# Kernel tuning notes

Measured on AMD Instinct MI355X. Metric: run time of the kernel, lower is better.

Reference implementation:

```python
import jax, jax.numpy as jnp
import numpy as np

IN_F = 512
OUT_F = 512
LMAX = 4
M = (LMAX + 1) ** 2  # 25
BATCH = 4096


def _expand_index():
    # l repeated (2l+1) times: [0, 1,1,1, 2,2,2,2,2, ...]
    return np.concatenate([np.full(2 * l + 1, l, dtype=np.int32) for l in range(LMAX + 1)])


def setup_inputs() -> dict:
    key = jax.random.key(0)
    k1, k2 = jax.random.split(key)
    bound = 1.0 / np.sqrt(IN_F)
    x = jax.random.normal(k1, (BATCH, IN_F * M, 1), dtype=jnp.float32)
    weight = jax.random.uniform(k2, (LMAX + 1, OUT_F, IN_F), dtype=jnp.float32,
                                minval=-bound, maxval=bound)
    bias = jnp.zeros((OUT_F,), dtype=jnp.float32)
    return {"input": x, "weight": weight, "bias": bias}


def reference(input, weight, bias):
    B = input.shape[0]
    idx = jnp.asarray(_expand_index())
    # gather-expand shared per-l weight to per-m weight: [M, out, in]
    w = weight[idx]
    # 'b (i m) n -> b m (i n)' with n=1  => [B, M, in]
    xi = input[..., 0].reshape(B, IN_F, M).transpose(0, 2, 1)
    # batched per-m linear: [B, M, out]
    out = jnp.einsum('bmi,moi->bmo', xi, w)
    # bias added only to the m=0 (l=0 scalar) component
    out = out.at[:, 0, :].add(bias)
    # 'b (m n) o -> b (o m) n' with n=1 => [B, out*M, 1]
    return out.transpose(0, 2, 1).reshape(B, OUT_F * M, 1)
```

## Files before the change

kernel.cpp:

```cpp
#include <hip/hip_runtime.h>
#include <hip/hip_bf16.h>


typedef __bf16 bf16x8 __attribute__((ext_vector_type(8)));
typedef float floatx4 __attribute__((ext_vector_type(4)));
typedef unsigned short ushort_t;
typedef unsigned short ushortx4 __attribute__((ext_vector_type(4)));

#define ROW_F 12800
#define SROW  72
#define LDS_USH (400 * 72)

__device__ __forceinline__ ushort_t f2bf(float f) {
    __hip_bfloat16 h = __float2bfloat16(f);
    return __builtin_bit_cast(ushort_t, h);
}

__global__ void cvt_w_kernel(const float* __restrict__ w, ushort_t* __restrict__ wb) {
    int i = (blockIdx.x * 256 + threadIdx.x) * 4;
    floatx4 v = *reinterpret_cast<const floatx4*>(w + i);
    ushortx4 h;
    h.x = f2bf(v[0]); h.y = f2bf(v[1]); h.z = f2bf(v[2]); h.w = f2bf(v[3]);
    *reinterpret_cast<ushortx4*>(wb + i) = h;
}

__global__ __launch_bounds__(512, 2) void irrep_kernel(
        const float* __restrict__ x, const ushort_t* __restrict__ wb,
        const float* __restrict__ bias, float* __restrict__ out) {
    __shared__ __align__(16) ushort_t Asm[LDS_USH];

    const int tid  = threadIdx.x;
    const int lane = tid & 63;
    const int wv   = tid >> 6;
    const int lr   = lane & 15;
    const int lh   = lane >> 4;

    const int d     = blockIdx.x;
    const int o     = (d & 7) * 128 + (d >> 3);
    const int btile = o >> 2;
    const int ctile = o & 3;
    const int b0    = btile * 16;
    const int o0    = ctile * 128;
    const int ow    = o0 + wv * 16;

    constexpr int LOF[25] = {0,1,1,1,2,2,2,2,2,3,3,3,3,3,3,3,4,4,4,4,4,4,4,4,4};

    floatx4 acc[25];
#pragma unroll
    for (int m = 0; m < 25; ++m) acc[m] = (floatx4){0.f, 0.f, 0.f, 0.f};

    floatx4 vbuf[13];

    auto prefetch = [&](int step) {
#pragma unroll
        for (int it = 0; it < 13; ++it) {
            int idx = tid + it * 512;
            if (idx < 6400) {
                int bb = idx / 400;
                int p  = idx - bb * 400;
                vbuf[it] = *reinterpret_cast<const floatx4*>(
                    x + (size_t)(b0 + bb) * ROW_F + (size_t)step * 1600 + p * 4);
            }
        }
    };

    auto scatter = [&]() {
#pragma unroll
        for (int it = 0; it < 13; ++it) {
            int idx = tid + it * 512;
            if (idx < 6400) {
                int bb = idx / 400;
                int p  = idx - bb * 400;
#pragma unroll
                for (int u = 0; u < 4; ++u) {
                    int q = p * 4 + u;
                    int i = q / 25;
                    int m = q - i * 25;
                    Asm[(m * 16 + bb) * SROW + (i ^ ((m & 7) << 3))] = f2bf(vbuf[it][u]);
                }
            }
        }
    };

    prefetch(0);
#pragma unroll 1
    for (int step = 0; step < 8; ++step) {
        __syncthreads();
        scatter();
        __syncthreads();
        if (step < 7) prefetch(step + 1);
        const int k0 = step * 64;
#pragma unroll
        for (int ks = 0; ks < 2; ++ks) {
            bf16x8 bfr[5];
#pragma unroll
            for (int l = 0; l < 5; ++l)
                bfr[l] = *reinterpret_cast<const bf16x8*>(
                    wb + (size_t)(l * 512 + ow + lr) * 512 + k0 + ks * 32 + lh * 8);
#pragma unroll
            for (int m = 0; m < 25; ++m) {
                const bf16x8 a = *reinterpret_cast<const bf16x8*>(
                    &Asm[(m * 16 + lr) * SROW + ((ks * 32 + lh * 8) ^ ((m & 7) << 3))]);
                acc[m] = __builtin_amdgcn_mfma_f32_16x16x32_bf16(a, bfr[LOF[m]], acc[m], 0, 0, 0);
            }
        }
    }

    {
        float bv = bias[ow + lr];
#pragma unroll
        for (int r = 0; r < 4; ++r) acc[0][r] += bv;
    }

    float* ep = reinterpret_cast<float*>(Asm);
    constexpr int EPROW = 404;
#pragma unroll 1
    for (int pass = 0; pass < 4; ++pass) {
        __syncthreads();
        if ((wv >> 1) == pass) {
            const int half = wv & 1;
            float* epw = ep + half * (16 * EPROW);
#pragma unroll
            for (int m = 0; m < 25; ++m) {
#pragma unroll
                for (int r = 0; r < 4; ++r) {
                    int bl = lh * 4 + r;
                    epw[bl * EPROW + lr * 25 + m] = acc[m][r];
                }
            }
        }
        __syncthreads();
        for (int idx = tid; idx < 3200; idx += 512) {
            int half = idx / 1600;
            int rem  = idx - half * 1600;
            int bl   = rem / 100;
            int q4   = rem - bl * 100;
            floatx4 v = *reinterpret_cast<const floatx4*>(
                &ep[half * (16 * EPROW) + bl * EPROW + q4 * 4]);
            *reinterpret_cast<floatx4*>(
                out + (size_t)(b0 + bl) * ROW_F
                    + (size_t)(o0 + (pass * 2 + half) * 16) * 25 + q4 * 4) = v;
        }
    }
}

extern "C" void kernel_launch(void* const* d_in, const int* in_sizes, int n_in,
                              void* d_out, int out_size, void* d_ws, size_t ws_size,
                              hipStream_t stream) {
    const float* x    = (const float*)d_in[0];
    const float* w    = (const float*)d_in[1];
    const float* bias = (const float*)d_in[2];
    float* outp       = (float*)d_out;
    ushort_t* wb      = (ushort_t*)d_ws;

    cvt_w_kernel<<<1280, 256, 0, stream>>>(w, wb);
    irrep_kernel<<<1024, 512, 0, stream>>>(x, wb, bias, outp);
}
```

Baseline: 272.0 us.

## Restructure irrep GEMM into 10-wave blocks with double-buffered LDS and per-wave m-groups

Splits each block's work so every wave owns a group of five m components across two 16-wide output slices, instead of all 25 m for one slice. Blocks now cover 64 output features with 640 threads and 2048 blocks. The input is staged through a double-buffered LDS tile with a new swizzle and 8-element vector stores, so the next chunk's global loads and scatter overlap the MFMAs, with one barrier per step. The idea is to cut per-wave accumulator registers for higher occupancy and to hide load latency. The cost is that each input tile is loaded twice (once per output half), and the epilogue takes more barriers.

After: 453.3 us. 66.7% more time.

```diff
diff --git a/kernel.cpp b/kernel.cpp
--- a/kernel.cpp
+++ b/kernel.cpp
@@ -2,18 +2,24 @@
 #include <hip/hip_bf16.h>
 
 
-typedef __bf16 bf16x8 __attribute__((ext_vector_type(8)));
+typedef __bf16 bf16x8v __attribute__((ext_vector_type(8)));
 typedef float floatx4 __attribute__((ext_vector_type(4)));
 typedef unsigned short ushort_t;
 typedef unsigned short ushortx4 __attribute__((ext_vector_type(4)));
+typedef unsigned short ushortx8 __attribute__((ext_vector_type(8)));
 
 #define ROW_F 12800
-#define SROW  72
-#define LDS_USH (400 * 72)
+#define BUF_USH 16064
 
 __device__ __forceinline__ ushort_t f2bf(float f) {
     __hip_bfloat16 h = __float2bfloat16(f);
     return __builtin_bit_cast(ushort_t, h);
+}
+
+__device__ __forceinline__ int row_ush(int row) {
+    int m = row >> 4;
+    int t = (m & 8) ? ((15 - m) & 7) : (m & 7);
+    return row * 40 + t * 8;
 }
 
 __global__ void cvt_w_kernel(const float* __restrict__ w, ushort_t* __restrict__ wb) {
@@ -24,123 +30,142 @@
     *reinterpret_cast<ushortx4*>(wb + i) = h;
 }
 
-__global__ __launch_bounds__(512, 2) void irrep_kernel(
+__global__ __launch_bounds__(640, 3) void irrep_kernel(
         const float* __restrict__ x, const ushort_t* __restrict__ wb,
         const float* __restrict__ bias, float* __restrict__ out) {
-    __shared__ __align__(16) ushort_t Asm[LDS_USH];
+    __shared__ __align__(16) ushort_t Asm[2 * BUF_USH];
 
-    const int tid  = threadIdx.x;
-    const int lane = tid & 63;
-    const int wv   = tid >> 6;
-    const int lr   = lane & 15;
-    const int lh   = lane >> 4;
+    const int tid = threadIdx.x, lane = tid & 63, wv = tid >> 6;
+    const int lr = lane & 15, lh = lane >> 4;
 
-    const int d     = blockIdx.x;
-    const int o     = (d & 7) * 128 + (d >> 3);
-    const int btile = o >> 2;
-    const int ctile = o & 3;
-    const int b0    = btile * 16;
-    const int o0    = ctile * 128;
-    const int ow    = o0 + wv * 16;
+    const int hw = blockIdx.x;
+    const int sib = (hw >> 3) & 7;
+    const int btile = (hw & 7) | ((hw >> 6) << 3);
+    const int b0 = btile * 16, o0 = sib * 64;
 
-    constexpr int LOF[25] = {0,1,1,1,2,2,2,2,2,3,3,3,3,3,3,3,4,4,4,4,4,4,4,4,4};
+    const int g = wv % 5;
+    const int po = wv / 5;
+    const int ob = o0 + po * 32;
 
-    floatx4 acc[25];
+    const float* rdp[3]; int wro[3];
 #pragma unroll
-    for (int m = 0; m < 25; ++m) acc[m] = (floatx4){0.f, 0.f, 0.f, 0.f};
+    for (int ba = 0; ba < 3; ++ba) {
+        int bi = tid + ba * 640;
+        if (bi < 1600) {
+            int bb = bi / 100, r = bi - bb * 100;
+            int m = r % 25, io = r / 25;
+            rdp[ba] = x + (size_t)(b0 + bb) * ROW_F + io * 8 * 25 + m;
+            wro[ba] = row_ush(m * 16 + bb) + io * 8;
+        } else { rdp[ba] = x; wro[ba] = 0; }
+    }
 
-    floatx4 vbuf[13];
-
-    auto prefetch = [&](int step) {
+    float vbuf[3][8];
+    auto issue_all = [&]() {
 #pragma unroll
-        for (int it = 0; it < 13; ++it) {
-            int idx = tid + it * 512;
-            if (idx < 6400) {
-                int bb = idx / 400;
-                int p  = idx - bb * 400;
-                vbuf[it] = *reinterpret_cast<const floatx4*>(
-                    x + (size_t)(b0 + bb) * ROW_F + (size_t)step * 1600 + p * 4);
-            }
+        for (int ba = 0; ba < 3; ++ba) if (ba * 640 + tid < 1600) {
+#pragma unroll
+            for (int j = 0; j < 8; ++j) vbuf[ba][j] = rdp[ba][j * 25];
+            rdp[ba] += 800;
+        }
+    };
+    auto scat = [&](int buf) {
+#pragma unroll
+        for (int ba = 0; ba < 3; ++ba) if (ba * 640 + tid < 1600) {
+            ushortx8 w8;
+#pragma unroll
+            for (int j = 0; j < 8; ++j) w8[j] = f2bf(vbuf[ba][j]);
+            *reinterpret_cast<ushortx8*>(&Asm[buf * BUF_USH + wro[ba]]) = w8;
         }
     };
 
-    auto scatter = [&]() {
+    const ushort_t* wbp[3][2];
+    {
+        constexpr int LV[5][3] = {{0,1,2},{2,3,3},{3,3,3},{3,4,4},{4,4,4}};
 #pragma unroll
-        for (int it = 0; it < 13; ++it) {
-            int idx = tid + it * 512;
-            if (idx < 6400) {
-                int bb = idx / 400;
-                int p  = idx - bb * 400;
+        for (int li = 0; li < 3; ++li)
 #pragma unroll
-                for (int u = 0; u < 4; ++u) {
-                    int q = p * 4 + u;
-                    int i = q / 25;
-                    int m = q - i * 25;
-                    Asm[(m * 16 + bb) * SROW + (i ^ ((m & 7) << 3))] = f2bf(vbuf[it][u]);
-                }
-            }
-        }
-    };
-
-    prefetch(0);
-#pragma unroll 1
-    for (int step = 0; step < 8; ++step) {
-        __syncthreads();
-        scatter();
-        __syncthreads();
-        if (step < 7) prefetch(step + 1);
-        const int k0 = step * 64;
-#pragma unroll
-        for (int ks = 0; ks < 2; ++ks) {
-            bf16x8 bfr[5];
-#pragma unroll
-            for (int l = 0; l < 5; ++l)
-                bfr[l] = *reinterpret_cast<const bf16x8*>(
-                    wb + (size_t)(l * 512 + ow + lr) * 512 + k0 + ks * 32 + lh * 8);
-#pragma unroll
-            for (int m = 0; m < 25; ++m) {
-                const bf16x8 a = *reinterpret_cast<const bf16x8*>(
-                    &Asm[(m * 16 + lr) * SROW + ((ks * 32 + lh * 8) ^ ((m & 7) << 3))]);
-                acc[m] = __builtin_amdgcn_mfma_f32_16x16x32_bf16(a, bfr[LOF[m]], acc[m], 0, 0, 0);
-            }
-        }
+            for (int of = 0; of < 2; ++of)
+                wbp[li][of] = wb + (size_t)(LV[g][li] * 512 + ob + of * 16 + lr) * 512 + lh * 8;
     }
 
-    {
-        float bv = bias[ow + lr];
+    int aoff[5];
 #pragma unroll
-        for (int r = 0; r < 4; ++r) acc[0][r] += bv;
+    for (int mm = 0; mm < 5; ++mm)
+        aoff[mm] = row_ush((g * 5 + mm) * 16 + lr) + lh * 8;
+
+    floatx4 acc[5][2];
+#pragma unroll
+    for (int mm = 0; mm < 5; ++mm)
+#pragma unroll
+        for (int of = 0; of < 2; ++of) acc[mm][of] = (floatx4){0.f, 0.f, 0.f, 0.f};
+
+    issue_all();
+    scat(0);
+    __syncthreads();
+    int cur = 0;
+
+#pragma unroll 1
+    for (int s = 0; s < 16; ++s) {
+        if (s < 15) issue_all();
+        bf16x8v bfr[3][2];
+#pragma unroll
+        for (int li = 0; li < 3; ++li)
+#pragma unroll
+            for (int of = 0; of < 2; ++of) {
+                bfr[li][of] = *reinterpret_cast<const bf16x8v*>(wbp[li][of]);
+                wbp[li][of] += 32;
+            }
+        bf16x8v afr[5];
+#pragma unroll
+        for (int mm = 0; mm < 5; ++mm)
+            afr[mm] = *reinterpret_cast<const bf16x8v*>(&Asm[cur * BUF_USH + aoff[mm]]);
+#pragma unroll
+        for (int Gc = 0; Gc < 5; ++Gc) if (g == Gc) {
+            constexpr int IDXT[5][5] = {{0,1,1,1,2},{0,0,0,0,1},{0,0,0,0,0},{0,1,1,1,1},{0,0,0,0,0}};
+#pragma unroll
+            for (int mm = 0; mm < 5; ++mm)
+#pragma unroll
+                for (int of = 0; of < 2; ++of)
+                    acc[mm][of] = __builtin_amdgcn_mfma_f32_16x16x32_bf16(
+                        afr[mm], bfr[IDXT[Gc][mm]][of], acc[mm][of], 0, 0, 0);
+        }
+        if (s < 15) scat(cur ^ 1);
+        __syncthreads();
+        cur ^= 1;
+    }
+
+    if (g == 0) {
+        float bv0 = bias[ob + lr], bv1 = bias[ob + 16 + lr];
+#pragma unroll
+        for (int r = 0; r < 4; ++r) { acc[0][0][r] += bv0; acc[0][1][r] += bv1; }
     }
 
     float* ep = reinterpret_cast<float*>(Asm);
-    constexpr int EPROW = 404;
+    constexpr int EPROW = 1608;
 #pragma unroll 1
-    for (int pass = 0; pass < 4; ++pass) {
-        __syncthreads();
-        if ((wv >> 1) == pass) {
-            const int half = wv & 1;
-            float* epw = ep + half * (16 * EPROW);
+    for (int p = 0; p < 4; ++p) {
+        if (lh == p) {
 #pragma unroll
-            for (int m = 0; m < 25; ++m) {
+            for (int of = 0; of < 2; ++of) {
+                int cb = (po * 32 + of * 16 + lr) * 25 + g * 5;
 #pragma unroll
-                for (int r = 0; r < 4; ++r) {
-                    int bl = lh * 4 + r;
-                    epw[bl * EPROW + lr * 25 + m] = acc[m][r];
+                for (int rr = 0; rr < 4; ++rr) {
+                    float* dst = ep + rr * EPROW + cb;
+                    dst[0] = acc[0][of][rr]; dst[1] = acc[1][of][rr];
+                    dst[2] = acc[2][of][rr]; dst[3] = acc[3][of][rr];
+                    dst[4] = acc[4][of][rr];
                 }
             }
         }
         __syncthreads();
-        for (int idx = tid; idx < 3200; idx += 512) {
-            int half = idx / 1600;
-            int rem  = idx - half * 1600;
-            int bl   = rem / 100;
-            int q4   = rem - bl * 100;
-            floatx4 v = *reinterpret_cast<const floatx4*>(
-                &ep[half * (16 * EPROW) + bl * EPROW + q4 * 4]);
+#pragma unroll 1
+        for (int idx = tid; idx < 1600; idx += 640) {
+            int rr = idx / 400, c4 = idx - rr * 400;
+            floatx4 v = *reinterpret_cast<const floatx4*>(ep + rr * EPROW + c4 * 4);
             *reinterpret_cast<floatx4*>(
-                out + (size_t)(b0 + bl) * ROW_F
-                    + (size_t)(o0 + (pass * 2 + half) * 16) * 25 + q4 * 4) = v;
+                out + (size_t)(b0 + p * 4 + rr) * ROW_F + o0 * 25 + c4 * 4) = v;
         }
+        __syncthreads();
     }
 }
 
@@ -154,5 +179,5 @@
     ushort_t* wb      = (ushort_t*)d_ws;
 
     cvt_w_kernel<<<1280, 256, 0, stream>>>(w, wb);
-    irrep_kernel<<<1024, 512, 0, stream>>>(x, wb, bias, outp);
+    irrep_kernel<<<2048, 640, 0, stream>>>(x, wb, bias, outp);
 }
```
